# Kernel optimization log

Hardware: AMD Instinct MI355X
Metric: run time of the kernel (lower is better)

The kernel has to match this reference:

```python
import jax, jax.numpy as jnp
import numpy as np

D_MODEL, N_HEADS, N_AGENTS = 1024, 16, 64
HEAD_DIM = D_MODEL // N_HEADS
B, N = 4, 4096


def setup_inputs() -> dict:
    key = jax.random.key(0)
    ks = jax.random.split(key, 12)
    hs = HEAD_DIM
    inp = {
        "q": jax.random.normal(ks[0], (B, N_HEADS, N, hs), jnp.float32),
        "k": jax.random.normal(ks[1], (B, N_HEADS, N, hs), jnp.float32),
        "v": jax.random.normal(ks[2], (B, N_HEADS, N, hs), jnp.float32),
        # per-head linear layers (torch nn.Linear: y = x @ W.T + b)
        "Wq": jax.random.normal(ks[3], (hs, hs), jnp.float32) / np.sqrt(hs),
        "bq": jnp.zeros((hs,), jnp.float32),
        "Wk": jax.random.normal(ks[4], (hs, hs), jnp.float32) / np.sqrt(hs),
        "bk": jnp.zeros((hs,), jnp.float32),
        "Wv": jax.random.normal(ks[5], (hs, hs), jnp.float32) / np.sqrt(hs),
        "bv": jnp.zeros((hs,), jnp.float32),
        "Wo": jax.random.normal(ks[6], (D_MODEL, D_MODEL), jnp.float32) / np.sqrt(D_MODEL),
        "bo": jnp.zeros((D_MODEL,), jnp.float32),
        "agent_tokens": jax.random.normal(ks[7], (1, N_HEADS, N_AGENTS, hs), jnp.float32),
    }
    return inp


def reference(q, k, v, Wq, bq, Wk, bk, Wv, bv, Wo, bo, agent_tokens):
    Bq, nh, N_, hs = q.shape
    scale = 1.0 / np.sqrt(hs).astype(np.float32)
    agents = jnp.broadcast_to(agent_tokens, (Bq, nh, N_AGENTS, hs))
    q_agents = jnp.einsum("bhad,ed->bhae", agents, Wq) + bq   # [B,nh,A,hs]
    k_agents = jnp.einsum("bhnd,ed->bhne", k, Wk) + bk        # [B,nh,N,hs]
    v_agents = jnp.einsum("bhnd,ed->bhne", v, Wv) + bv        # [B,nh,N,hs]
    # stage 1: agents attend to keys/values
    scores1 = jnp.einsum("bhad,bhnd->bhan", q_agents, k_agents) * scale
    scores1 = jax.nn.softmax(scores1, axis=-1)
    context1 = jnp.einsum("bhan,bhnd->bhad", scores1, v_agents)  # [B,nh,A,hs]
    # stage 2: queries attend to agent context
    scores2 = jnp.einsum("bhnd,bhad->bhna", q, context1) * scale
    scores2 = jax.nn.softmax(scores2, axis=-1)
    context2 = jnp.einsum("bhna,bhad->bhnd", scores2, context1)  # [B,nh,N,hs]
    context2 = context2.transpose(0, 2, 1, 3).reshape(Bq, N_, nh * hs)
    output = context2 @ Wo.T + bo  # dropout is identity in eval
    return output, scores2
```

## Files before the change

### kernel.cpp

```cpp
#include <hip/hip_runtime.h>

#define NB 4
#define NH 16
#define NN 4096
#define HS 64
#define NA 64
#define DM 1024
#define NBH (NB*NH)
#define SCALE 0.125f

typedef __attribute__((ext_vector_type(8))) short bf16x8;
typedef __attribute__((ext_vector_type(4))) float f32x4;

__device__ __forceinline__ unsigned short f2bf(float f) {
  unsigned u = __float_as_uint(f);
  u += 0x7FFF + ((u >> 16) & 1);
  return (unsigned short)(u >> 16);
}

__device__ __forceinline__ void gload_lds16(const void* g, void* l) {
  __builtin_amdgcn_global_load_lds(
      (const __attribute__((address_space(1))) unsigned int*)g,
      (__attribute__((address_space(3))) unsigned int*)l, 16, 0, 0);
}

__device__ __forceinline__ void dot44(float (&c)[4][4], const float4 (&a)[4], const float4 (&b)[4]) {
#pragma unroll
  for (int i = 0; i < 4; ++i)
#pragma unroll
    for (int j = 0; j < 4; ++j) {
      c[i][j] = fmaf(a[i].x, b[j].x, c[i][j]);
      c[i][j] = fmaf(a[i].y, b[j].y, c[i][j]);
      c[i][j] = fmaf(a[i].z, b[j].z, c[i][j]);
      c[i][j] = fmaf(a[i].w, b[j].w, c[i][j]);
    }
}

__global__ __launch_bounds__(256) void k0_fold(
    const float* __restrict__ agents, const float* __restrict__ Wq,
    const float* __restrict__ bq, const float* __restrict__ Wk,
    unsigned short* __restrict__ foldqbf) {
  const int h = blockIdx.x, tid = threadIdx.x;
  const int tn = tid & 15, tm = tid >> 4;
  __shared__ float AG[64][68];
  __shared__ float WB[64][68];
  __shared__ float QA[64][68];
  __shared__ float WKT[64][68];
  for (int i = tid; i < 1024; i += 256) {
    const int r = i >> 4, c4 = (i & 15) * 4;
    *(float4*)&AG[r][c4] = *(const float4*)(agents + h * 4096 + r * 64 + c4);
    *(float4*)&WB[r][c4] = *(const float4*)(Wq + r * 64 + c4);
    const float4 f = *(const float4*)(Wk + r * 64 + c4);
    WKT[c4 + 0][r] = f.x; WKT[c4 + 1][r] = f.y;
    WKT[c4 + 2][r] = f.z; WKT[c4 + 3][r] = f.w;
  }
  __syncthreads();
  {
    const float4 bb = *(const float4*)(bq + tn * 4);
    float acc[4][4];
#pragma unroll
    for (int i = 0; i < 4; ++i) {
      acc[i][0] = bb.x; acc[i][1] = bb.y; acc[i][2] = bb.z; acc[i][3] = bb.w;
    }
    for (int d4 = 0; d4 < 64; d4 += 4) {
      float4 a4[4], b4[4];
#pragma unroll
      for (int i = 0; i < 4; ++i) a4[i] = *(const float4*)&AG[tm * 4 + i][d4];
#pragma unroll
      for (int j = 0; j < 4; ++j) b4[j] = *(const float4*)&WB[tn * 4 + j][d4];
      dot44(acc, a4, b4);
    }
#pragma unroll
    for (int i = 0; i < 4; ++i)
      *(float4*)&QA[tm * 4 + i][tn * 4] =
          make_float4(acc[i][0], acc[i][1], acc[i][2], acc[i][3]);
  }
  __syncthreads();
  {
    float acc[4][4] = {};
    for (int e4 = 0; e4 < 64; e4 += 4) {
      float4 a4[4], b4[4];
#pragma unroll
      for (int i = 0; i < 4; ++i) a4[i] = *(const float4*)&QA[tm * 4 + i][e4];
#pragma unroll
      for (int j = 0; j < 4; ++j) b4[j] = *(const float4*)&WKT[tn * 4 + j][e4];
      dot44(acc, a4, b4);
    }
#pragma unroll
    for (int i = 0; i < 4; ++i) {
      ushort4 o;
      o.x = f2bf(acc[i][0] * SCALE); o.y = f2bf(acc[i][1] * SCALE);
      o.z = f2bf(acc[i][2] * SCALE); o.w = f2bf(acc[i][3] * SCALE);
      *(ushort4*)(foldqbf + h * 4096 + (tm * 4 + i) * 64 + tn * 4) = o;
    }
  }
}

__global__ __launch_bounds__(256) void k2_mfma(
    const float* __restrict__ kraw, const float* __restrict__ vraw,
    const unsigned short* __restrict__ foldqbf,
    float* __restrict__ pctx, float* __restrict__ psum) {
  __shared__ unsigned short FQ[64 * 72];
  __shared__ unsigned short KN[64 * 72];
  __shared__ unsigned short VT[64 * 72];
  __shared__ unsigned short ES[64 * 72];
  const int chunk = blockIdx.x, bh = blockIdx.y, h = bh & 15;
  const int tid = threadIdx.x;
  const int lane = tid & 63, w = tid >> 6;
  const int l15 = lane & 15, lg = lane >> 4;

  const size_t kvbase = ((size_t)bh * NN + chunk * 256) * HS;
  float4 kreg[4], vreg[4];
#pragma unroll
  for (int i0 = 0; i0 < 4; ++i0) {
    const int i = tid + i0 * 256;
    kreg[i0] = *(const float4*)(kraw + kvbase + (size_t)i * 4);
    vreg[i0] = *(const float4*)(vraw + kvbase + (size_t)i * 4);
  }

  for (int i = tid; i < 512; i += 256) {
    const int a = i >> 3, d8 = (i & 7) * 8;
    *(uint4*)&FQ[a * 72 + d8] = *(const uint4*)(foldqbf + h * 4096 + a * 64 + d8);
  }

  f32x4 ctx[4];
#pragma unroll
  for (int df = 0; df < 4; ++df) ctx[df] = (f32x4){0.f, 0.f, 0.f, 0.f};
  f32x4 pacc = (f32x4){0.f, 0.f, 0.f, 0.f};
  const short one_bf = (short)0x3F80;
  const bf16x8 ones = {one_bf, one_bf, one_bf, one_bf, one_bf, one_bf, one_bf, one_bf};

  for (int t = 0; t < 4; ++t) {
    __syncthreads();
#pragma unroll
    for (int i0 = 0; i0 < 4; ++i0) {
      const int i = tid + i0 * 256;
      const int n = i >> 4, d4 = (i & 15) * 4;
      const float4 f = kreg[i0];
      const unsigned klo = f2bf(f.x) | ((unsigned)f2bf(f.y) << 16);
      const unsigned khi = f2bf(f.z) | ((unsigned)f2bf(f.w) << 16);
      *(uint2*)&KN[n * 72 + d4] = make_uint2(klo, khi);
      const float4 g = vreg[i0];
      const int nn = n ^ (8 * (i & 7));
      VT[(d4 + 0) * 72 + nn] = f2bf(g.x);
      VT[(d4 + 1) * 72 + nn] = f2bf(g.y);
      VT[(d4 + 2) * 72 + nn] = f2bf(g.z);
      VT[(d4 + 3) * 72 + nn] = f2bf(g.w);
    }
    if (t < 3) {
#pragma unroll
      for (int i0 = 0; i0 < 4; ++i0) {
        const int i = tid + i0 * 256;
        kreg[i0] = *(const float4*)(kraw + kvbase + (size_t)(t + 1) * 4096 + (size_t)i * 4);
        vreg[i0] = *(const float4*)(vraw + kvbase + (size_t)(t + 1) * 4096 + (size_t)i * 4);
      }
    }
    __syncthreads();
    const bf16x8 af0 = *(const bf16x8*)&KN[(w * 16 + l15) * 72 + lg * 8];
    const bf16x8 af1 = *(const bf16x8*)&KN[(w * 16 + l15) * 72 + 32 + lg * 8];
    f32x4 sacc[4];
#pragma unroll
    for (int afr = 0; afr < 4; ++afr) {
      sacc[afr] = (f32x4){0.f, 0.f, 0.f, 0.f};
      const bf16x8 b0 = *(const bf16x8*)&FQ[(afr * 16 + l15) * 72 + lg * 8];
      const bf16x8 b1 = *(const bf16x8*)&FQ[(afr * 16 + l15) * 72 + 32 + lg * 8];
      sacc[afr] = __builtin_amdgcn_mfma_f32_16x16x32_bf16(af0, b0, sacc[afr], 0, 0, 0);
      sacc[afr] = __builtin_amdgcn_mfma_f32_16x16x32_bf16(af1, b1, sacc[afr], 0, 0, 0);
    }
#pragma unroll
    for (int afr = 0; afr < 4; ++afr) {
      const unsigned e0 = f2bf(__expf(sacc[afr][0])) | ((unsigned)f2bf(__expf(sacc[afr][1])) << 16);
      const unsigned e1 = f2bf(__expf(sacc[afr][2])) | ((unsigned)f2bf(__expf(sacc[afr][3])) << 16);
      *(uint2*)&ES[(afr * 16 + l15) * 72 + w * 16 + lg * 4] = make_uint2(e0, e1);
    }
    __syncthreads();
    const bf16x8 ea0 = *(const bf16x8*)&ES[(w * 16 + l15) * 72 + lg * 8];
    const bf16x8 ea1 = *(const bf16x8*)&ES[(w * 16 + l15) * 72 + 32 + lg * 8];
    pacc = __builtin_amdgcn_mfma_f32_16x16x32_bf16(ea0, ones, pacc, 0, 0, 0);
    pacc = __builtin_amdgcn_mfma_f32_16x16x32_bf16(ea1, ones, pacc, 0, 0, 0);
#pragma unroll
    for (int df = 0; df < 4; ++df) {
      const int d = df * 16 + l15;
      const int sw = 8 * ((d >> 2) & 7);
      const bf16x8 vb0 = *(const bf16x8*)&VT[d * 72 + ((lg * 8) ^ sw)];
      const bf16x8 vb1 = *(const bf16x8*)&VT[d * 72 + ((32 + lg * 8) ^ sw)];
      ctx[df] = __builtin_amdgcn_mfma_f32_16x16x32_bf16(ea0, vb0, ctx[df], 0, 0, 0);
      ctx[df] = __builtin_amdgcn_mfma_f32_16x16x32_bf16(ea1, vb1, ctx[df], 0, 0, 0);
    }
  }
  const size_t pbase = ((size_t)bh * 16 + chunk) * 4096;
#pragma unroll
  for (int df = 0; df < 4; ++df)
#pragma unroll
    for (int r = 0; r < 4; ++r)
      pctx[pbase + (w * 16 + lg * 4 + r) * 64 + df * 16 + l15] = ctx[df][r];
  if (l15 == 0) {
#pragma unroll
    for (int r = 0; r < 4; ++r)
      psum[((size_t)bh * 16 + chunk) * 64 + w * 16 + lg * 4 + r] = pacc[r];
  }
}

__global__ __launch_bounds__(256) void k3_reduce(
    const float* __restrict__ pctx, const float* __restrict__ psum,
    const float* __restrict__ Wv, const float* __restrict__ bv,
    unsigned short* __restrict__ c1nbf) {
  const int bh = blockIdx.x, aq = blockIdx.y;
  const int tid = threadIdx.x;
  const int tn = tid & 15, tm = tid >> 4;
  __shared__ float sinv[16];
  __shared__ float CR[16][68];
  __shared__ float WT[64][68];
  if (tid < 16) {
    const int a = aq * 16 + tid;
    float s = 0.f;
#pragma unroll 4
    for (int c = 0; c < 16; ++c) s += psum[((size_t)bh * 16 + c) * 64 + a];
    sinv[tid] = 1.0f / s;
  }
  for (int i = tid; i < 1024; i += 256) {
    const int e = i >> 4, d4 = (i & 15) * 4;
    const float4 f = *(const float4*)(Wv + e * 64 + d4);
    WT[d4 + 0][e] = f.x; WT[d4 + 1][e] = f.y;
    WT[d4 + 2][e] = f.z; WT[d4 + 3][e] = f.w;
  }
  __syncthreads();
  {
    const int al = tid >> 4, d4 = (tid & 15) * 4;
    const size_t base = (size_t)bh * 16 * 4096 + (size_t)(aq * 16 + al) * 64 + d4;
    float4 s = make_float4(0.f, 0.f, 0.f, 0.f);
#pragma unroll 4
    for (int c = 0; c < 16; ++c) {
      const float4 f = *(const float4*)(pctx + base + (size_t)c * 4096);
      s.x += f.x; s.y += f.y; s.z += f.z; s.w += f.w;
    }
    const float si = sinv[al];
    CR[al][d4 + 0] = s.x * si; CR[al][d4 + 1] = s.y * si;
    CR[al][d4 + 2] = s.z * si; CR[al][d4 + 3] = s.w * si;
  }
  __syncthreads();
  float acc[4];
  const float4 bb = *(const float4*)(bv + tn * 4);
  acc[0] = bb.x; acc[1] = bb.y; acc[2] = bb.z; acc[3] = bb.w;
#pragma unroll 8
  for (int d = 0; d < 64; ++d) {
    const float a0 = CR[tm][d];
    const float4 wv4 = *(const float4*)&WT[d][tn * 4];
    acc[0] = fmaf(a0, wv4.x, acc[0]);
    acc[1] = fmaf(a0, wv4.y, acc[1]);
    acc[2] = fmaf(a0, wv4.z, acc[2]);
    acc[3] = fmaf(a0, wv4.w, acc[3]);
  }
  ushort4 o;
  o.x = f2bf(acc[0]); o.y = f2bf(acc[1]); o.z = f2bf(acc[2]); o.w = f2bf(acc[3]);
  *(ushort4*)(c1nbf + (size_t)bh * 4096 + (size_t)(aq * 16 + tm) * 64 + tn * 4) = o;
}

__global__ __launch_bounds__(256) void kG(
    const unsigned short* __restrict__ c1nbf, const float* __restrict__ Wo,
    unsigned short* __restrict__ GT) {
  const int et = blockIdx.x;
  const int bh = blockIdx.y, h = bh & 15;
  const int e0 = et * 256;
  __shared__ unsigned short WoS[256 * 72];
  __shared__ unsigned short C1S[64 * 72];
  const int tid = threadIdx.x;
  const int lane = tid & 63, w = tid >> 6;
  const int l15 = lane & 15, lg = lane >> 4;
  for (int i = tid; i < 4096; i += 256) {
    const int e = i >> 4, d4 = (i & 15) * 4;
    const float4 f = *(const float4*)(Wo + (size_t)(e0 + e) * DM + h * 64 + d4);
    ushort4 o;
    o.x = f2bf(f.x); o.y = f2bf(f.y); o.z = f2bf(f.z); o.w = f2bf(f.w);
    *(ushort4*)&WoS[e * 72 + d4] = o;
  }
  for (int i = tid; i < 512; i += 256) {
    const int a = i >> 3, d8 = (i & 7) * 8;
    *(uint4*)&C1S[a * 72 + d8] =
        *(const uint4*)(c1nbf + (size_t)bh * 4096 + a * 64 + d8);
  }
  __syncthreads();
  bf16x8 b0[4], b1[4];
#pragma unroll
  for (int at = 0; at < 4; ++at) {
    b0[at] = *(const bf16x8*)&C1S[(at * 16 + l15) * 72 + lg * 8];
    b1[at] = *(const bf16x8*)&C1S[(at * 16 + l15) * 72 + 32 + lg * 8];
  }
#pragma unroll
  for (int et16 = 0; et16 < 4; ++et16) {
    const int erow = w * 64 + et16 * 16 + l15;
    const bf16x8 a0 = *(const bf16x8*)&WoS[erow * 72 + lg * 8];
    const bf16x8 a1 = *(const bf16x8*)&WoS[erow * 72 + 32 + lg * 8];
#pragma unroll
    for (int at = 0; at < 4; ++at) {
      f32x4 acc = (f32x4){0.f, 0.f, 0.f, 0.f};
      acc = __builtin_amdgcn_mfma_f32_16x16x32_bf16(a0, b0[at], acc, 0, 0, 0);
      acc = __builtin_amdgcn_mfma_f32_16x16x32_bf16(a1, b1[at], acc, 0, 0, 0);
      const size_t gbase =
          ((size_t)bh * 1024 + e0 + w * 64 + et16 * 16 + lg * 4) * 64 + at * 16 + l15;
#pragma unroll
      for (int r = 0; r < 4; ++r) GT[gbase + (size_t)r * 64] = f2bf(acc[r]);
    }
  }
}

__global__ __launch_bounds__(256) void k4_mfma(
    const float* __restrict__ q, const unsigned short* __restrict__ c1nbf,
    float* __restrict__ scores2, unsigned short* __restrict__ P2bf) {
  __shared__ unsigned short C1N[64 * 72];
  __shared__ unsigned short PS[64 * 72];
  const int bh = blockIdx.y;
  const int n0 = blockIdx.x * 64;
  const int tid = threadIdx.x;
  const int lane = tid & 63, w = tid >> 6;
  const int l15 = lane & 15, lg = lane >> 4;

  for (int i = tid; i < 512; i += 256) {
    const int a = i >> 3, d8 = (i & 7) * 8;
    *(uint4*)&C1N[a * 72 + d8] =
        *(const uint4*)(c1nbf + (size_t)bh * 4096 + a * 64 + d8);
  }
  const float* qr = q + ((size_t)bh * NN + n0 + w * 16 + l15) * HS;
  const float4 qa = *(const float4*)(qr + lg * 8);
  const float4 qb = *(const float4*)(qr + lg * 8 + 4);
  const float4 qc = *(const float4*)(qr + 32 + lg * 8);
  const float4 qd = *(const float4*)(qr + 32 + lg * 8 + 4);
  bf16x8 af0, af1;
  af0[0] = (short)f2bf(qa.x * SCALE); af0[1] = (short)f2bf(qa.y * SCALE);
  af0[2] = (short)f2bf(qa.z * SCALE); af0[3] = (short)f2bf(qa.w * SCALE);
  af0[4] = (short)f2bf(qb.x * SCALE); af0[5] = (short)f2bf(qb.y * SCALE);
  af0[6] = (short)f2bf(qb.z * SCALE); af0[7] = (short)f2bf(qb.w * SCALE);
  af1[0] = (short)f2bf(qc.x * SCALE); af1[1] = (short)f2bf(qc.y * SCALE);
  af1[2] = (short)f2bf(qc.z * SCALE); af1[3] = (short)f2bf(qc.w * SCALE);
  af1[4] = (short)f2bf(qd.x * SCALE); af1[5] = (short)f2bf(qd.y * SCALE);
  af1[6] = (short)f2bf(qd.z * SCALE); af1[7] = (short)f2bf(qd.w * SCALE);
  __syncthreads();

  f32x4 sacc[4];
#pragma unroll
  for (int afr = 0; afr < 4; ++afr) {
    sacc[afr] = (f32x4){0.f, 0.f, 0.f, 0.f};
    const bf16x8 b0 = *(const bf16x8*)&C1N[(afr * 16 + l15) * 72 + lg * 8];
    const bf16x8 b1 = *(const bf16x8*)&C1N[(afr * 16 + l15) * 72 + 32 + lg * 8];
    sacc[afr] = __builtin_amdgcn_mfma_f32_16x16x32_bf16(af0, b0, sacc[afr], 0, 0, 0);
    sacc[afr] = __builtin_amdgcn_mfma_f32_16x16x32_bf16(af1, b1, sacc[afr], 0, 0, 0);
  }
  float p[4][4];
#pragma unroll
  for (int r = 0; r < 4; ++r) {
    float m = fmaxf(fmaxf(sacc[0][r], sacc[1][r]), fmaxf(sacc[2][r], sacc[3][r]));
#pragma unroll
    for (int off = 1; off < 16; off <<= 1) m = fmaxf(m, __shfl_xor(m, off));
    float s = 0.f;
#pragma unroll
    for (int afr = 0; afr < 4; ++afr) {
      p[afr][r] = __expf(sacc[afr][r] - m);
      s += p[afr][r];
    }
#pragma unroll
    for (int off = 1; off < 16; off <<= 1) s += __shfl_xor(s, off);
    const float inv = 1.0f / s;
    const size_t srow = ((size_t)bh * NN + n0 + w * 16 + lg * 4 + r) * NA;
#pragma unroll
    for (int afr = 0; afr < 4; ++afr) {
      p[afr][r] *= inv;
      scores2[srow + afr * 16 + l15] = p[afr][r];
      PS[(w * 16 + lg * 4 + r) * 72 + afr * 16 + l15] = f2bf(p[afr][r]);
    }
  }
  const int prow = w * 16 + (lane >> 2);
  const int pch = (lane & 3) * 16;
  const uint4 v0 = *(const uint4*)&PS[prow * 72 + pch];
  const uint4 v1 = *(const uint4*)&PS[prow * 72 + pch + 8];
  unsigned short* gp = P2bf + ((size_t)bh * NN + n0 + prow) * NA + pch;
  *(uint4*)gp = v0;
  *(uint4*)(gp + 8) = v1;
}

__global__ __launch_bounds__(512, 1) void k5_mfma(
    const unsigned short* __restrict__ P2, const unsigned short* __restrict__ GT,
    const float* __restrict__ bo, float* __restrict__ out) {
  __shared__ unsigned short As[2][256 * 64];
  __shared__ unsigned short Bs[2][256 * 64];
  const int tid = threadIdx.x;
  const int lane = tid & 63;
  const int w = tid >> 6;
  const int wr = w >> 2, wc = w & 3;
  const int l15 = lane & 15, lg = lane >> 4;
  const int mblk = blockIdx.x;
  const int b16 = (mblk >> 4) * 16;
  const int nloc0 = (mblk & 15) * 256;
  const int e0 = blockIdx.y * 256;

  const int srow8 = lane >> 3;
  const int sslot = ((lane & 7) ^ srow8) << 4;

  f32x4 acc[8][4] = {{{0.f}}};

#define K5_STAGE(T, BUF)                                                       \
  {                                                                            \
    const char* Ab = (const char*)(P2 + ((size_t)(b16 + (T)) * NN + nloc0) * NA); \
    const char* Gb = (const char*)(GT + ((size_t)(b16 + (T)) * 1024 + e0) * NA);  \
    _Pragma("unroll")                                                          \
    for (int j = 0; j < 4; ++j) {                                              \
      const int rb = j * 64 + w * 8;                \
      const int r = rb + srow8;                                                \
      gload_lds16(Ab + (size_t)r * 128 + sslot,                                \
                  (char*)As[BUF] + rb * 128 + lane * 16);                      \
      gload_lds16(Gb + (size_t)r * 128 + sslot,                                \
                  (char*)Bs[BUF] + rb * 128 + lane * 16);                      \
    }                                                                          \
  }

  K5_STAGE(0, 0);
  K5_STAGE(1, 1);
  for (int t = 0; t < 16; ++t) {
    if (t < 15) {
      asm volatile("s_waitcnt vmcnt(8)" ::: "memory");
    } else {
      asm volatile("s_waitcnt vmcnt(0)" ::: "memory");
    }
    __builtin_amdgcn_sched_barrier(0);
    __builtin_amdgcn_s_barrier();
    __builtin_amdgcn_sched_barrier(0);
    const char* Ac = (const char*)As[t & 1];
    const char* Bc = (const char*)Bs[t & 1];
#pragma unroll
    for (int ks = 0; ks < 2; ++ks) {
      bf16x8 af[8], bfr[4];
#pragma unroll
      for (int m = 0; m < 8; ++m) {
        const int r = wr * 128 + m * 16 + l15;
        const int byt = (ks * 64 + lg * 16) ^ ((r & 7) << 4);
        af[m] = *(const bf16x8*)(Ac + r * 128 + byt);
      }
#pragma unroll
      for (int n = 0; n < 4; ++n) {
        const int r = wc * 64 + n * 16 + l15;
        const int byt = (ks * 64 + lg * 16) ^ ((r & 7) << 4);
        bfr[n] = *(const bf16x8*)(Bc + r * 128 + byt);
      }
#pragma unroll
      for (int m = 0; m < 8; ++m)
#pragma unroll
        for (int n = 0; n < 4; ++n)
          acc[m][n] = __builtin_amdgcn_mfma_f32_16x16x32_bf16(af[m], bfr[n], acc[m][n], 0, 0, 0);
    }
    __builtin_amdgcn_sched_barrier(0);
    __builtin_amdgcn_s_barrier();
    __builtin_amdgcn_sched_barrier(0);
    if (t + 2 < 16) K5_STAGE(t + 2, t & 1);
  }
#undef K5_STAGE

  const size_t mrow0 = (size_t)(b16 >> 4) * NN + nloc0;
#pragma unroll
  for (int m = 0; m < 8; ++m) {
    const size_t row0 = mrow0 + wr * 128 + m * 16 + lg * 4;
#pragma unroll
    for (int n = 0; n < 4; ++n) {
      const int c = e0 + wc * 64 + n * 16 + l15;
      const float bias = bo[c];
#pragma unroll
      for (int r = 0; r < 4; ++r)
        out[(row0 + r) * DM + c] = acc[m][n][r] + bias;
    }
  }
}

extern "C" void kernel_launch(void* const* d_in, const int* in_sizes, int n_in,
                              void* d_out, int out_size, void* d_ws, size_t ws_size,
                              hipStream_t stream) {
  (void)in_sizes; (void)n_in; (void)out_size; (void)ws_size;
  const float* q  = (const float*)d_in[0];
  const float* k  = (const float*)d_in[1];
  const float* v  = (const float*)d_in[2];
  const float* Wq = (const float*)d_in[3];
  const float* bq = (const float*)d_in[4];
  const float* Wk = (const float*)d_in[5];
  const float* bk = (const float*)d_in[6];
  const float* Wv = (const float*)d_in[7];
  const float* bv = (const float*)d_in[8];
  const float* Wo = (const float*)d_in[9];
  const float* bo = (const float*)d_in[10];
  const float* ag = (const float*)d_in[11];
  (void)bk;

  float* out0 = (float*)d_out;
  float* scores2 = out0 + (size_t)NB * NN * DM;

  float* ws = (float*)d_ws;
  unsigned short* foldqbf = (unsigned short*)ws;
  unsigned short* c1nbf = (unsigned short*)(ws + 65536);
  float* psum = ws + 65536 + 262144;
  float* pctx = psum + 65536;
  unsigned short* GT = (unsigned short*)pctx;
  unsigned short* P2bf = (unsigned short*)(pctx + 4194304);

  k0_fold<<<NH, 256, 0, stream>>>(ag, Wq, bq, Wk, foldqbf);
  k2_mfma<<<dim3(16, NBH), 256, 0, stream>>>(k, v, foldqbf, pctx, psum);
  k3_reduce<<<dim3(NBH, 4), 256, 0, stream>>>(pctx, psum, Wv, bv, c1nbf);
  kG<<<dim3(4, NBH), 256, 0, stream>>>(c1nbf, Wo, GT);
  k4_mfma<<<dim3(NN / 64, NBH), 256, 0, stream>>>(q, c1nbf, scores2, P2bf);
  k5_mfma<<<dim3(NB * NN / 256, DM / 256), 512, 0, stream>>>(P2bf, GT, bo, out0);
}
```

Before: 145.4 us.

## Interleave prefetch loads with quartered MFMA phases in output projection GEMM

Splits each K-step of the final output-projection GEMM into four quadrant phases (M-half by N-half). LDS fragment reads, global-to-LDS prefetch of the next-next stage, and MFMA blocks alternate across these phases, separated by barriers, with s_setprio raised around the MFMAs. The aim is to hide LDS and global load latency behind matrix math instead of issuing all loads and then all MFMAs. In exchange it adds many more workgroup barriers per step and a more fragile buffer-reuse ordering, since the prefetch writes into the buffer currently being read.

Measured after the change: 146.0 us. About the same (+0.4%).

```diff
diff --git a/kernel.cpp b/kernel.cpp
--- a/kernel.cpp
+++ b/kernel.cpp
@@ -394,64 +394,127 @@
 
   const int srow8 = lane >> 3;
   const int sslot = ((lane & 7) ^ srow8) << 4;
+  const int rbB = ((w >> 2) * 64) + (w & 3) * 8;
 
   f32x4 acc[8][4] = {{{0.f}}};
 
-#define K5_STAGE(T, BUF)                                                       \
+#define K5_SPA(T, BUF, RB)                                                     \
   {                                                                            \
     const char* Ab = (const char*)(P2 + ((size_t)(b16 + (T)) * NN + nloc0) * NA); \
-    const char* Gb = (const char*)(GT + ((size_t)(b16 + (T)) * 1024 + e0) * NA);  \
-    _Pragma("unroll")                                                          \
-    for (int j = 0; j < 4; ++j) {                                              \
-      const int rb = j * 64 + w * 8;                \
-      const int r = rb + srow8;                                                \
-      gload_lds16(Ab + (size_t)r * 128 + sslot,                                \
-                  (char*)As[BUF] + rb * 128 + lane * 16);                      \
-      gload_lds16(Gb + (size_t)r * 128 + sslot,                                \
-                  (char*)Bs[BUF] + rb * 128 + lane * 16);                      \
-    }                                                                          \
-  }
-
-  K5_STAGE(0, 0);
-  K5_STAGE(1, 1);
+    const int rb = (RB);                                                       \
+    gload_lds16(Ab + (size_t)(rb + srow8) * 128 + sslot,                       \
+                (char*)As[BUF] + rb * 128 + lane * 16);                        \
+  }
+#define K5_SPB(T, BUF, RB)                                                     \
+  {                                                                            \
+    const char* Gb = (const char*)(GT + ((size_t)(b16 + (T)) * 1024 + e0) * NA); \
+    const int rb = (RB);                                                       \
+    gload_lds16(Gb + (size_t)(rb + srow8) * 128 + sslot,                       \
+                (char*)Bs[BUF] + rb * 128 + lane * 16);                        \
+  }
+#define K5_STAGE_FULL(T, BUF)                                                  \
+  {                                                                            \
+    K5_SPA(T, BUF, w * 8); K5_SPA(T, BUF, 64 + w * 8);                         \
+    K5_SPA(T, BUF, 128 + w * 8); K5_SPA(T, BUF, 192 + w * 8);                  \
+    K5_SPB(T, BUF, w * 8); K5_SPB(T, BUF, 64 + w * 8);                         \
+    K5_SPB(T, BUF, 128 + w * 8); K5_SPB(T, BUF, 192 + w * 8);                  \
+  }
+
+#define K5_BAR()                        \
+  __builtin_amdgcn_sched_barrier(0);    \
+  __builtin_amdgcn_s_barrier();         \
+  __builtin_amdgcn_sched_barrier(0);
+
+#define K5_LGKM0()                                      \
+  asm volatile("s_waitcnt lgkmcnt(0)" ::: "memory");    \
+  __builtin_amdgcn_sched_barrier(0);
+
+#define K5_RD_AF(DST, MH)                                               \
+  _Pragma("unroll") for (int m = 0; m < 4; ++m) {                       \
+    const int r = wr * 128 + (MH) * 64 + m * 16 + l15;                  \
+    _Pragma("unroll") for (int ks = 0; ks < 2; ++ks) {                  \
+      const int byt = (ks * 64 + lg * 16) ^ ((r & 7) << 4);             \
+      DST[m][ks] = *(const bf16x8*)(Ac + r * 128 + byt);                \
+    }                                                                   \
+  }
+#define K5_RD_BF(NH2)                                                   \
+  _Pragma("unroll") for (int n = 0; n < 2; ++n) {                       \
+    const int r = wc * 64 + (NH2) * 32 + n * 16 + l15;                  \
+    _Pragma("unroll") for (int ks = 0; ks < 2; ++ks) {                  \
+      const int byt = (ks * 64 + lg * 16) ^ ((r & 7) << 4);             \
+      bfv[n][ks] = *(const bf16x8*)(Bc + r * 128 + byt);                \
+    }                                                                   \
+  }
+#define K5_MFMA_Q(AF, MH, NH2)                                                   \
+  __builtin_amdgcn_s_setprio(1);                                                 \
+  _Pragma("unroll") for (int ks = 0; ks < 2; ++ks)                               \
+  _Pragma("unroll") for (int m = 0; m < 4; ++m)                                  \
+  _Pragma("unroll") for (int n = 0; n < 2; ++n)                                  \
+    acc[(MH) * 4 + m][(NH2) * 2 + n] = __builtin_amdgcn_mfma_f32_16x16x32_bf16(  \
+        AF[m][ks], bfv[n][ks], acc[(MH) * 4 + m][(NH2) * 2 + n], 0, 0, 0);       \
+  __builtin_amdgcn_s_setprio(0);
+
+  K5_STAGE_FULL(0, 0);
+  K5_STAGE_FULL(1, 1);
+  asm volatile("s_waitcnt vmcnt(8)" ::: "memory");
+  K5_BAR();
+
   for (int t = 0; t < 16; ++t) {
-    if (t < 15) {
+    const int c = t & 1;
+    const char* Ac = (const char*)As[c];
+    const char* Bc = (const char*)Bs[c];
+    bf16x8 af0_[4][2], af1_[4][2], bfv[2][2];
+
+    K5_RD_AF(af0_, 0);
+    K5_RD_BF(0);
+    K5_BAR();
+    K5_LGKM0();
+    K5_MFMA_Q(af0_, 0, 0);
+    K5_BAR();
+
+    K5_RD_AF(af1_, 1);
+    if (t < 14) {
+      K5_SPA(t + 2, c, w * 8);
+      K5_SPA(t + 2, c, 128 + w * 8);
+      K5_SPB(t + 2, c, rbB);
+      K5_SPB(t + 2, c, 128 + rbB);
+    }
+    K5_BAR();
+    K5_LGKM0();
+    K5_MFMA_Q(af1_, 1, 0);
+    K5_BAR();
+
+    K5_RD_BF(1);
+    if (t < 14) {
+      K5_SPA(t + 2, c, 64 + w * 8);
+      K5_SPA(t + 2, c, 192 + w * 8);
+    }
+    K5_BAR();
+    K5_LGKM0();
+    K5_MFMA_Q(af1_, 1, 1);
+    K5_BAR();
+
+    if (t < 14) {
+      K5_SPB(t + 2, c, 32 + rbB);
+      K5_SPB(t + 2, c, 160 + rbB);
+    }
+    K5_BAR();
+    K5_MFMA_Q(af0_, 0, 1);
+    if (t < 14) {
       asm volatile("s_waitcnt vmcnt(8)" ::: "memory");
-    } else {
+    } else if (t == 14) {
       asm volatile("s_waitcnt vmcnt(0)" ::: "memory");
     }
-    __builtin_amdgcn_sched_barrier(0);
-    __builtin_amdgcn_s_barrier();
-    __builtin_amdgcn_sched_barrier(0);
-    const char* Ac = (const char*)As[t & 1];
-    const char* Bc = (const char*)Bs[t & 1];
-#pragma unroll
-    for (int ks = 0; ks < 2; ++ks) {
-      bf16x8 af[8], bfr[4];
-#pragma unroll
-      for (int m = 0; m < 8; ++m) {
-        const int r = wr * 128 + m * 16 + l15;
-        const int byt = (ks * 64 + lg * 16) ^ ((r & 7) << 4);
-        af[m] = *(const bf16x8*)(Ac + r * 128 + byt);
-      }
-#pragma unroll
-      for (int n = 0; n < 4; ++n) {
-        const int r = wc * 64 + n * 16 + l15;
-        const int byt = (ks * 64 + lg * 16) ^ ((r & 7) << 4);
-        bfr[n] = *(const bf16x8*)(Bc + r * 128 + byt);
-      }
-#pragma unroll
-      for (int m = 0; m < 8; ++m)
-#pragma unroll
-        for (int n = 0; n < 4; ++n)
-          acc[m][n] = __builtin_amdgcn_mfma_f32_16x16x32_bf16(af[m], bfr[n], acc[m][n], 0, 0, 0);
-    }
-    __builtin_amdgcn_sched_barrier(0);
-    __builtin_amdgcn_s_barrier();
-    __builtin_amdgcn_sched_barrier(0);
-    if (t + 2 < 16) K5_STAGE(t + 2, t & 1);
-  }
-#undef K5_STAGE
+    K5_BAR();
+  }
+#undef K5_SPA
+#undef K5_SPB
+#undef K5_STAGE_FULL
+#undef K5_BAR
+#undef K5_LGKM0
+#undef K5_RD_AF
+#undef K5_RD_BF
+#undef K5_MFMA_Q
 
   const size_t mrow0 = (size_t)(b16 >> 4) * NN + nloc0;
 #pragma unroll
```

## Shrink k5 output tile, drop double buffering for higher occupancy

Applied to the files above, without the earlier changes.

The final projection GEMM now uses 256x128 output tiles instead of 256x256, which doubles the grid to 512 blocks. Shared memory drops to single-buffered A/B tiles and launch bounds allow four blocks per CU, so more waves can hide latency. In exchange, the explicit two-stage global-to-LDS prefetch pipeline is removed in favour of plain load/sync/compute/sync. The A tile is also reloaded twice as often across output columns.

Result: faster. 141.8 us (-2.5%).

```diff
diff --git a/kernel.cpp b/kernel.cpp
--- a/kernel.cpp
+++ b/kernel.cpp
@@ -377,89 +377,73 @@
   *(uint4*)(gp + 8) = v1;
 }
 
-__global__ __launch_bounds__(512, 1) void k5_mfma(
+__global__ __launch_bounds__(512, 4) void k5_mfma(
     const unsigned short* __restrict__ P2, const unsigned short* __restrict__ GT,
     const float* __restrict__ bo, float* __restrict__ out) {
-  __shared__ unsigned short As[2][256 * 64];
-  __shared__ unsigned short Bs[2][256 * 64];
+  __shared__ unsigned short As[256 * 64];
+  __shared__ unsigned short Bs[128 * 64];
   const int tid = threadIdx.x;
   const int lane = tid & 63;
   const int w = tid >> 6;
   const int wr = w >> 2, wc = w & 3;
   const int l15 = lane & 15, lg = lane >> 4;
-  const int mblk = blockIdx.x;
-  const int b16 = (mblk >> 4) * 16;
-  const int nloc0 = (mblk & 15) * 256;
-  const int e0 = blockIdx.y * 256;
+  const int rp = blockIdx.x;
+  const int e0 = blockIdx.y * 128;
+  const int b16 = (rp >> 4) * 16;
+  const int nloc0 = (rp & 15) * 256;
 
   const int srow8 = lane >> 3;
   const int sslot = ((lane & 7) ^ srow8) << 4;
 
-  f32x4 acc[8][4] = {{{0.f}}};
-
-#define K5_STAGE(T, BUF)                                                       \
-  {                                                                            \
-    const char* Ab = (const char*)(P2 + ((size_t)(b16 + (T)) * NN + nloc0) * NA); \
-    const char* Gb = (const char*)(GT + ((size_t)(b16 + (T)) * 1024 + e0) * NA);  \
-    _Pragma("unroll")                                                          \
-    for (int j = 0; j < 4; ++j) {                                              \
-      const int rb = j * 64 + w * 8;                \
-      const int r = rb + srow8;                                                \
-      gload_lds16(Ab + (size_t)r * 128 + sslot,                                \
-                  (char*)As[BUF] + rb * 128 + lane * 16);                      \
-      gload_lds16(Gb + (size_t)r * 128 + sslot,                                \
-                  (char*)Bs[BUF] + rb * 128 + lane * 16);                      \
-    }                                                                          \
-  }
-
-  K5_STAGE(0, 0);
-  K5_STAGE(1, 1);
+  f32x4 acc[8][2] = {{{0.f}}};
+
   for (int t = 0; t < 16; ++t) {
-    if (t < 15) {
-      asm volatile("s_waitcnt vmcnt(8)" ::: "memory");
-    } else {
-      asm volatile("s_waitcnt vmcnt(0)" ::: "memory");
-    }
-    __builtin_amdgcn_sched_barrier(0);
-    __builtin_amdgcn_s_barrier();
-    __builtin_amdgcn_sched_barrier(0);
-    const char* Ac = (const char*)As[t & 1];
-    const char* Bc = (const char*)Bs[t & 1];
+    const char* Ab = (const char*)(P2 + ((size_t)(b16 + t) * NN + nloc0) * NA);
+    const char* Gb = (const char*)(GT + ((size_t)(b16 + t) * 1024 + e0) * NA);
+#pragma unroll
+    for (int j = 0; j < 4; ++j) {
+      const int rb = j * 64 + w * 8;
+      gload_lds16(Ab + (size_t)(rb + srow8) * 128 + sslot,
+                  (char*)As + rb * 128 + lane * 16);
+    }
+#pragma unroll
+    for (int j = 0; j < 2; ++j) {
+      const int rb = j * 64 + w * 8;
+      gload_lds16(Gb + (size_t)(rb + srow8) * 128 + sslot,
+                  (char*)Bs + rb * 128 + lane * 16);
+    }
+    __syncthreads();
 #pragma unroll
     for (int ks = 0; ks < 2; ++ks) {
-      bf16x8 af[8], bfr[4];
+      bf16x8 af[8], bfr[2];
 #pragma unroll
       for (int m = 0; m < 8; ++m) {
         const int r = wr * 128 + m * 16 + l15;
         const int byt = (ks * 64 + lg * 16) ^ ((r & 7) << 4);
-        af[m] = *(const bf16x8*)(Ac + r * 128 + byt);
+        af[m] = *(const bf16x8*)((const char*)As + r * 128 + byt);
       }
 #pragma unroll
-      for (int n = 0; n < 4; ++n) {
-        const int r = wc * 64 + n * 16 + l15;
+      for (int n = 0; n < 2; ++n) {
+        const int r = wc * 32 + n * 16 + l15;
         const int byt = (ks * 64 + lg * 16) ^ ((r & 7) << 4);
-        bfr[n] = *(const bf16x8*)(Bc + r * 128 + byt);
+        bfr[n] = *(const bf16x8*)((const char*)Bs + r * 128 + byt);
       }
 #pragma unroll
       for (int m = 0; m < 8; ++m)
 #pragma unroll
-        for (int n = 0; n < 4; ++n)
+        for (int n = 0; n < 2; ++n)
           acc[m][n] = __builtin_amdgcn_mfma_f32_16x16x32_bf16(af[m], bfr[n], acc[m][n], 0, 0, 0);
     }
-    __builtin_amdgcn_sched_barrier(0);
-    __builtin_amdgcn_s_barrier();
-    __builtin_amdgcn_sched_barrier(0);
-    if (t + 2 < 16) K5_STAGE(t + 2, t & 1);
-  }
-#undef K5_STAGE
+    __syncthreads();
+  }
 
   const size_t mrow0 = (size_t)(b16 >> 4) * NN + nloc0;
 #pragma unroll
   for (int m = 0; m < 8; ++m) {
     const size_t row0 = mrow0 + wr * 128 + m * 16 + lg * 4;
 #pragma unroll
-    for (int n = 0; n < 4; ++n) {
-      const int c = e0 + wc * 64 + n * 16 + l15;
+    for (int n = 0; n < 2; ++n) {
+      const int c = e0 + wc * 32 + n * 16 + l15;
       const float bias = bo[c];
 #pragma unroll
       for (int r = 0; r < 4; ++r)
@@ -502,5 +486,5 @@
   k3_reduce<<<dim3(NBH, 4), 256, 0, stream>>>(pctx, psum, Wv, bv, c1nbf);
   kG<<<dim3(4, NBH), 256, 0, stream>>>(c1nbf, Wo, GT);
   k4_mfma<<<dim3(NN / 64, NBH), 256, 0, stream>>>(q, c1nbf, scores2, P2bf);
-  k5_mfma<<<dim3(NB * NN / 256, DM / 256), 512, 0, stream>>>(P2bf, GT, bo, out0);
-}
+  k5_mfma<<<dim3(64, 8), 512, 0, stream>>>(P2bf, GT, bo, out0);
+}
```
